# Performance work log

Measured on AMD Instinct MI355X. Metric: run time of the kernel, lower is better.

## Reference

```python
import jax, jax.numpy as jnp
import numpy as np

N_NODES = 25000
N_EDGES = 100000
N_GRAPHS = 1000
DIM = 64
NUM_FEAT = 14
EDGE_FEAT = 4
HIDDEN_EDGE = 128
NUM_OUT = 1
NUM_CONV_STEPS = 3
SET2SET_STEPS = 3
NEG_SLOPE = 0.01


def leaky_relu(x):
    return jnp.where(x > 0, x, NEG_SLOPE * x)


def setup_inputs() -> dict:
    key = jax.random.key(0)
    ks = jax.random.split(key, 24)
    s = lambda fan_in: 1.0 / np.sqrt(fan_in)
    inp = {
        "x": jax.random.normal(ks[0], (N_NODES, NUM_FEAT), dtype=jnp.float32),
        "edge_index": jax.random.randint(ks[1], (2, N_EDGES), 0, N_NODES),
        "edge_attr": jax.random.uniform(ks[2], (N_EDGES, EDGE_FEAT), dtype=jnp.float32),
        "batch": jnp.sort(jax.random.randint(ks[3], (N_NODES,), 0, N_GRAPHS)),
        # lin0
        "lin0_w": jax.random.normal(ks[4], (DIM, NUM_FEAT), dtype=jnp.float32) * s(NUM_FEAT),
        "lin0_b": jnp.zeros((DIM,), dtype=jnp.float32),
        # edge-weight MLP: Linear(4,128) -> LeakyReLU -> Linear(128, DIM*DIM)
        "net_w1": jax.random.normal(ks[5], (HIDDEN_EDGE, EDGE_FEAT), dtype=jnp.float32) * s(EDGE_FEAT),
        "net_b1": jnp.zeros((HIDDEN_EDGE,), dtype=jnp.float32),
        "net_w2": jax.random.normal(ks[6], (DIM * DIM, HIDDEN_EDGE), dtype=jnp.float32) * s(HIDDEN_EDGE),
        "net_b2": jnp.zeros((DIM * DIM,), dtype=jnp.float32),
        # NNConv root weight + bias
        "conv_root": jax.random.normal(ks[7], (DIM, DIM), dtype=jnp.float32) * s(DIM),
        "conv_bias": jnp.zeros((DIM,), dtype=jnp.float32),
        # GRU (single layer), torch gate order r,z,n
        "gru_w_ih": jax.random.normal(ks[8], (3 * DIM, DIM), dtype=jnp.float32) * s(DIM),
        "gru_w_hh": jax.random.normal(ks[9], (3 * DIM, DIM), dtype=jnp.float32) * s(DIM),
        "gru_b_ih": jnp.zeros((3 * DIM,), dtype=jnp.float32),
        "gru_b_hh": jnp.zeros((3 * DIM,), dtype=jnp.float32),
        # Set2Set LSTM: input 2*DIM -> hidden DIM, torch gate order i,f,g,o
        "lstm_w_ih": jax.random.normal(ks[10], (4 * DIM, 2 * DIM), dtype=jnp.float32) * s(2 * DIM),
        "lstm_w_hh": jax.random.normal(ks[11], (4 * DIM, DIM), dtype=jnp.float32) * s(DIM),
        "lstm_b_ih": jnp.zeros((4 * DIM,), dtype=jnp.float32),
        "lstm_b_hh": jnp.zeros((4 * DIM,), dtype=jnp.float32),
        # final linear on [B, 2*DIM]
        "lin_w": jax.random.normal(ks[12], (NUM_OUT, 2 * DIM), dtype=jnp.float32) * s(2 * DIM),
        "lin_b": jnp.zeros((NUM_OUT,), dtype=jnp.float32),
    }
    return inp


def _forward(x, edge_index, edge_attr, batch,
             lin0_w, lin0_b, net_w1, net_b1, net_w2, net_b2,
             conv_root, conv_bias, gru_w_ih, gru_w_hh, gru_b_ih, gru_b_hh,
             lstm_w_ih, lstm_w_hh, lstm_b_ih, lstm_b_hh, lin_w, lin_b):
    src, dst = edge_index[0], edge_index[1]

    out = leaky_relu(x @ lin0_w.T + lin0_b)          # [N, DIM]
    h = out                                          # GRU hidden [N, DIM]

    # edge_attr is constant across conv steps -> dynamic weights computed once
    W_e = (leaky_relu(edge_attr @ net_w1.T + net_b1) @ net_w2.T + net_b2)
    W_e = W_e.reshape(N_EDGES, DIM, DIM)             # [E, DIM, DIM]

    deg = jax.ops.segment_sum(jnp.ones((N_EDGES,), dtype=x.dtype), dst,
                              num_segments=N_NODES)
    inv_deg = jnp.where(deg > 0, 1.0 / jnp.maximum(deg, 1.0), 0.0)[:, None]

    for _ in range(NUM_CONV_STEPS):
        # NNConv: gather -> per-edge matmul -> scatter-mean, plus root term
        msg = jnp.einsum('ed,edo->eo', out[src], W_e)                 # [E, DIM]
        aggr = jax.ops.segment_sum(msg, dst, num_segments=N_NODES) * inv_deg
        m = leaky_relu(aggr + out @ conv_root + conv_bias)
        # single-step GRU (torch equations, gate order r,z,n)
        gi = m @ gru_w_ih.T + gru_b_ih
        gh = h @ gru_w_hh.T + gru_b_hh
        i_r, i_z, i_n = jnp.split(gi, 3, axis=-1)
        h_r, h_z, h_n = jnp.split(gh, 3, axis=-1)
        r = jax.nn.sigmoid(i_r + h_r)
        z = jax.nn.sigmoid(i_z + h_z)
        n = jnp.tanh(i_n + r * h_n)
        h = (1.0 - z) * n + z * h
        out = h

    # Set2Set pooling (processing_steps=3)
    q_star = jnp.zeros((N_GRAPHS, 2 * DIM), dtype=x.dtype)
    hl = jnp.zeros((N_GRAPHS, DIM), dtype=x.dtype)
    cl = jnp.zeros((N_GRAPHS, DIM), dtype=x.dtype)
    for _ in range(SET2SET_STEPS):
        gates = q_star @ lstm_w_ih.T + lstm_b_ih + hl @ lstm_w_hh.T + lstm_b_hh
        gi, gf, gg, go = jnp.split(gates, 4, axis=-1)
        cl = jax.nn.sigmoid(gf) * cl + jax.nn.sigmoid(gi) * jnp.tanh(gg)
        hl = jax.nn.sigmoid(go) * jnp.tanh(cl)
        q = hl                                                         # [B, DIM]
        e = jnp.sum(out * q[batch], axis=-1)                           # [N]
        e_max = jax.ops.segment_max(e, batch, num_segments=N_GRAPHS)
        e_exp = jnp.exp(e - e_max[batch])
        denom = jax.ops.segment_sum(e_exp, batch, num_segments=N_GRAPHS)
        a = e_exp / denom[batch]                                       # segment softmax
        r_read = jax.ops.segment_sum(a[:, None] * out, batch,
                                     num_segments=N_GRAPHS)            # [B, DIM]
        q_star = jnp.concatenate([q, r_read], axis=-1)

    return q_star @ lin_w.T + lin_b                                    # [B, NUM_OUT]


def reference(x, edge_index, edge_attr, batch,
              lin0_w, lin0_b, net_w1, net_b1, net_w2, net_b2,
              conv_root, conv_bias, gru_w_ih, gru_w_hh, gru_b_ih, gru_b_hh,
              lstm_w_ih, lstm_w_hh, lstm_b_ih, lstm_b_hh, lin_w, lin_b):
    return _forward(x, edge_index, edge_attr, batch,
                    lin0_w, lin0_b, net_w1, net_b1, net_w2, net_b2,
                    conv_root, conv_bias, gru_w_ih, gru_w_hh, gru_b_ih, gru_b_hh,
                    lstm_w_ih, lstm_w_hh, lstm_b_ih, lstm_b_hh, lin_w, lin_b)
```

## Files before the change

### kernel.cpp

```cpp
#include <hip/hip_runtime.h>
#include <math.h>

#define N_NODES_C  25000
#define N_EDGES_C  100000
#define N_GRAPHS_C 1000
#define EPB 128

typedef __attribute__((ext_vector_type(8))) _Float16 f16x8;
typedef __attribute__((ext_vector_type(4))) float   f32x4;

__device__ __forceinline__ float lrelu(float x) { return x > 0.f ? x : 0.01f * x; }
__device__ __forceinline__ float sigm(float x)  { return 1.f / (1.f + __expf(-x)); }
__device__ __forceinline__ f32x4 MFH(f16x8 a, f16x8 b, f32x4 c) {
  return __builtin_amdgcn_mfma_f32_16x16x32_f16(a, b, c, 0, 0, 0);
}

__global__ __launch_bounds__(256) void lin0_kernel(const float* __restrict__ x,
                            const float* __restrict__ w, const float* __restrict__ b,
                            float* __restrict__ nodeF) {
  __shared__ float ws[64 * 15];
  __shared__ float bs[64];
  __shared__ float xr[4][16];
  const int tid = threadIdx.x;
  for (int i = tid; i < 896; i += 256) { int o = i / 14, j = i % 14; ws[o * 15 + j] = w[i]; }
  if (tid < 64) bs[tid] = b[tid];
  const int nl = tid >> 6, o = tid & 63;
  const int n = blockIdx.x * 4 + nl;
  if (o < 14 && n < N_NODES_C) xr[nl][o] = x[n * 14 + o];
  __syncthreads();
  if (n < N_NODES_C) {
    float s = bs[o];
#pragma unroll
    for (int j = 0; j < 14; ++j) s += xr[nl][j] * ws[o * 15 + j];
    nodeF[n * 64 + o] = lrelu(s);
  }
}

__global__ void deg_kernel(const int* __restrict__ ei, float* __restrict__ deg) {
  int e = blockIdx.x * blockDim.x + threadIdx.x;
  if (e < N_EDGES_C) atomicAdd(&deg[ei[N_EDGES_C + e]], 1.f);
}

__global__ void invdeg_kernel(float* __restrict__ deg) {
  int n = blockIdx.x * blockDim.x + threadIdx.x;
  if (n < N_NODES_C) { float v = deg[n]; deg[n] = v > 0.f ? 1.f / v : 0.f; }
}

__global__ void goff_kernel(const int* __restrict__ batch, int* __restrict__ goff) {
  int g = blockIdx.x * blockDim.x + threadIdx.x;
  if (g > N_GRAPHS_C) return;
  int lo = 0, hi = N_NODES_C;
  while (lo < hi) { int mid = (lo + hi) >> 1; if (batch[mid] < g) lo = mid + 1; else hi = mid; }
  goff[g] = lo;
}

__global__ void prep_gru_kernel(const float* __restrict__ conv_root,
                                const float* __restrict__ w_ih, const float* __restrict__ w_hh,
                                _Float16* __restrict__ Rtp,
                                _Float16* __restrict__ Wip, _Float16* __restrict__ Whp) {
  int i = blockIdx.x * 256 + threadIdx.x;
  if (i < 12288) {
    int j = i & 7, lane = (i >> 3) & 63, kc = (i >> 9) & 1, t = i >> 10;
    int o = t * 16 + (lane & 15), d = kc * 32 + (lane >> 4) * 8 + j;
    if (i < 4096) Rtp[i] = (_Float16)conv_root[d * 64 + o];
    Wip[i] = (_Float16)w_ih[o * 64 + d];
    Whp[i] = (_Float16)w_hh[o * 64 + d];
  }
}

__global__ __launch_bounds__(256) void prep_w2_kernel(
    const float* __restrict__ net_w2, const float* __restrict__ net_b2,
    _Float16* __restrict__ Wp, _Float16* __restrict__ B2p) {
  int i = blockIdx.x * 256 + threadIdx.x;
  {
    int j = i & 7, lane = (i >> 3) & 63, q = (i >> 9) & 3, p = (i >> 11) & 1;
    int oh = (i >> 12) & 1, d = i >> 13;
    int kci = q >> 1, ob = q & 1;
    int col = lane & 15, kg = lane >> 4;
    int o = oh * 32 + ob * 16 + col, h = (p * 2 + kci) * 32 + kg * 8 + j;
    Wp[i] = (_Float16)net_w2[((size_t)d * 64 + o) * 128 + h];
  }
  if (i < 4096) {
    int j = i & 7, lane = (i >> 3) & 63, kc2 = (i >> 9) & 1, ob = (i >> 10) & 1, oh = (i >> 11) & 1;
    int col = lane & 15, kg = lane >> 4;
    int o = oh * 32 + ob * 16 + col, d = kc2 * 32 + kg * 8 + j;
    B2p[i] = (_Float16)net_b2[d * 64 + o];
  }
}

__global__ __launch_bounds__(256, 3) void msg_kernel(
    const float* __restrict__ nodef,
    const int*   __restrict__ ei,
    const float* __restrict__ eattr,
    const float* __restrict__ net_w1,
    const float* __restrict__ net_b1,
    const _Float16* __restrict__ Wp,
    const _Float16* __restrict__ B2p,
    float* __restrict__ aggr)
{
  __shared__ _Float16 xs[64 * EPB];
  __shared__ _Float16 xsT[EPB * 64];
  __shared__ float    w1s[128 * 5];

  const int tid = threadIdx.x;
  const int e0 = blockIdx.x * EPB;

  if (tid < 128) {
    float4 wv = *(const float4*)(net_w1 + tid * 4);
    w1s[tid * 5 + 0] = wv.x; w1s[tid * 5 + 1] = wv.y;
    w1s[tid * 5 + 2] = wv.z; w1s[tid * 5 + 3] = wv.w;
    w1s[tid * 5 + 4] = net_b1[tid];
  }
  {
    const int e = tid >> 1, dh = (tid & 1) * 32;
    int ge = e0 + e;
    const int esw = (e & 7) << 3;
#pragma unroll
    for (int jb = 0; jb < 4; ++jb) {
      int d = dh + jb * 8;
      float4 v0, v1;
      if (ge < N_EDGES_C) {
        const float4* nf4 = (const float4*)(nodef + (size_t)ei[ge] * 64 + d);
        v0 = nf4[0]; v1 = nf4[1];
      } else {
        v0 = make_float4(0.f, 0.f, 0.f, 0.f); v1 = v0;
      }
      f16x8 pk;
      pk[0] = (_Float16)v0.x; pk[1] = (_Float16)v0.y; pk[2] = (_Float16)v0.z; pk[3] = (_Float16)v0.w;
      pk[4] = (_Float16)v1.x; pk[5] = (_Float16)v1.y; pk[6] = (_Float16)v1.z; pk[7] = (_Float16)v1.w;
      *(f16x8*)&xsT[e * 64 + (d ^ esw)] = pk;
#pragma unroll
      for (int j = 0; j < 8; ++j) xs[(d + j) * EPB + e] = pk[j];
    }
  }

  const int lane = tid & 63, wv = tid >> 6;
  const int e0w = (wv & 1) * 64;
  const int oh  = wv >> 1;
  const int col = lane & 15;
  const int kg  = lane >> 4;
  const int swz = (col & 7) << 3;

  __syncthreads();

  f32x4 acc[4][2];
#pragma unroll
  for (int eb = 0; eb < 4; ++eb) { acc[eb][0] = 0.f; acc[eb][1] = 0.f; }
#pragma unroll
  for (int ob = 0; ob < 2; ++ob)
#pragma unroll
    for (int kc2 = 0; kc2 < 2; ++kc2) {
      f16x8 b2f = *(const f16x8*)(B2p + oh * 2048 + ob * 1024 + kc2 * 512 + lane * 8);
#pragma unroll
      for (int eb = 0; eb < 4; ++eb) {
        f16x8 xf = *(const f16x8*)&xsT[(e0w + eb * 16 + col) * 64 + ((kc2 * 32 + kg * 8) ^ swz)];
        acc[eb][ob] = MFH(xf, b2f, acc[eb][ob]);
      }
    }

  const _Float16* wp_base = Wp + oh * 4096 + lane * 8;
#pragma unroll 1
  for (int p = 0; p < 2; ++p) {
    f16x8 Af[4][2];
    {
      float4 at[4];
#pragma unroll
      for (int eb = 0; eb < 4; ++eb) {
        int ge = e0 + e0w + eb * 16 + col;
        at[eb] = (ge < N_EDGES_C) ? *(const float4*)(eattr + (size_t)ge * 4)
                                  : make_float4(0.f, 0.f, 0.f, 0.f);
      }
#pragma unroll
      for (int kci = 0; kci < 2; ++kci) {
        float4 wr[8]; float wb[8];
#pragma unroll
        for (int j = 0; j < 8; ++j) {
          int hq = (p * 2 + kci) * 32 + kg * 8 + j;
          wr[j] = *(const float4*)&w1s[hq * 5];
          wb[j] = w1s[hq * 5 + 4];
        }
#pragma unroll
        for (int eb = 0; eb < 4; ++eb) {
          f16x8 F;
#pragma unroll
          for (int j = 0; j < 8; ++j) {
            float a = wb[j] + at[eb].x * wr[j].x + at[eb].y * wr[j].y
                            + at[eb].z * wr[j].z + at[eb].w * wr[j].w;
            F[j] = (_Float16)lrelu(a);
          }
          Af[eb][kci] = F;
        }
      }
    }

    const _Float16* wp_p = wp_base + p * 2048;
    f16x8 B0[4], B1[4];
#define LOADB(BUF, dd)                                                   \
  {                                                                      \
    const _Float16* b_ = wp_p + (size_t)(dd) * 8192;                     \
    BUF[0] = *(const f16x8*)(b_);                                        \
    BUF[1] = *(const f16x8*)(b_ + 512);                                  \
    BUF[2] = *(const f16x8*)(b_ + 1024);                                 \
    BUF[3] = *(const f16x8*)(b_ + 1536);                                 \
  }
#define SLAB(BUF, dd)                                                    \
  {                                                                      \
    _Pragma("unroll")                                                    \
    for (int eb = 0; eb < 4; ++eb) {                                     \
      unsigned int xu = *(const unsigned short*)&xs[(dd) * EPB + e0w + eb * 16 + col]; \
      unsigned int xr_ = (xu << 16) | xu;                                \
      union { unsigned int u[4]; f16x8 v; } X;                           \
      X.u[0] = xr_; X.u[1] = xr_; X.u[2] = xr_; X.u[3] = xr_;            \
      _Pragma("unroll")                                                  \
      for (int kci = 0; kci < 2; ++kci) {                                \
        f16x8 U = Af[eb][kci] * X.v;                                     \
        acc[eb][0] = MFH(U, BUF[kci * 2 + 0], acc[eb][0]);               \
        acc[eb][1] = MFH(U, BUF[kci * 2 + 1], acc[eb][1]);               \
      }                                                                  \
    }                                                                    \
  }
    LOADB(B0, 0);
#pragma unroll 1
    for (int d = 0; d < 64; d += 2) {
      LOADB(B1, d + 1);
      SLAB(B0, d);
      if (d + 2 < 64) LOADB(B0, d + 2);
      SLAB(B1, d + 1);
    }
#undef LOADB
#undef SLAB
  }

  const int o0w = oh * 32;
#pragma unroll
  for (int eb = 0; eb < 4; ++eb) {
#pragma unroll
    for (int r = 0; r < 4; ++r) {
      int e = e0w + eb * 16 + kg * 4 + r;
      int ge = e0 + e;
      if (ge < N_EDGES_C) {
        int dn = ei[N_EDGES_C + ge];
        atomicAdd(&aggr[(size_t)dn * 64 + o0w + col],      acc[eb][0][r]);
        atomicAdd(&aggr[(size_t)dn * 64 + o0w + 16 + col], acc[eb][1][r]);
      }
    }
  }
}

__global__ __launch_bounds__(256) void node_update_kernel(
    float* __restrict__ aggr, const float* __restrict__ invdeg,
    const _Float16* __restrict__ Rtp, const _Float16* __restrict__ Wip,
    const _Float16* __restrict__ Whp,
    const float* __restrict__ conv_bias,
    const float* __restrict__ b_ih, const float* __restrict__ b_hh,
    float* __restrict__ nodeF)
{
  __shared__ _Float16 ms[4][16 * 64];

  const int tid = threadIdx.x, lane = tid & 63, wv = tid >> 6;
  const int col = lane & 15, kg = lane >> 4;
  const int nwb = blockIdx.x * 64 + wv * 16;

  int arow = nwb + col; if (arow >= N_NODES_C) arow = N_NODES_C - 1;
  f16x8 nf[2];
#pragma unroll
  for (int kc = 0; kc < 2; ++kc) {
    f32x4 v0 = *(const f32x4*)(nodeF + (size_t)arow * 64 + kc * 32 + kg * 8);
    f32x4 v1 = *(const f32x4*)(nodeF + (size_t)arow * 64 + kc * 32 + kg * 8 + 4);
    f16x8 F;
#pragma unroll
    for (int j = 0; j < 4; ++j) { F[j] = (_Float16)v0[j]; F[4 + j] = (_Float16)v1[j]; }
    nf[kc] = F;
  }

  f32x4 racc[4];
#pragma unroll
  for (int t = 0; t < 4; ++t) racc[t] = conv_bias[t * 16 + col];
#pragma unroll
  for (int t = 0; t < 4; ++t)
#pragma unroll
    for (int kc = 0; kc < 2; ++kc)
      racc[t] = MFH(nf[kc], *(const f16x8*)(Rtp + t * 1024 + kc * 512 + lane * 8), racc[t]);

  float invd[4]; int nrow[4];
#pragma unroll
  for (int r = 0; r < 4; ++r) {
    int nn = nwb + kg * 4 + r; nrow[r] = nn;
    invd[r] = (nn < N_NODES_C) ? invdeg[nn] : 0.f;
  }
#pragma unroll
  for (int t = 0; t < 4; ++t) {
#pragma unroll
    for (int r = 0; r < 4; ++r) {
      int nn = nrow[r];
      float ag = 0.f;
      if (nn < N_NODES_C) {
        size_t idx = (size_t)nn * 64 + t * 16 + col;
        ag = aggr[idx];
        aggr[idx] = 0.f;
      }
      float mval = lrelu(ag * invd[r] + racc[t][r]);
      int nl = kg * 4 + r;
      int dsw = (t * 16 + col) ^ ((nl & 7) << 3);
      ms[wv][nl * 64 + dsw] = (_Float16)mval;
    }
  }
  __syncthreads();

  f16x8 ma[2];
#pragma unroll
  for (int kc = 0; kc < 2; ++kc)
    ma[kc] = *(const f16x8*)&ms[wv][col * 64 + ((kc * 32 + kg * 8) ^ ((col & 7) << 3))];

  f32x4 gi[12], gh[12];
#pragma unroll
  for (int t = 0; t < 12; ++t) { gi[t] = b_ih[t * 16 + col]; gh[t] = b_hh[t * 16 + col]; }
#pragma unroll
  for (int t = 0; t < 12; ++t)
#pragma unroll
    for (int kc = 0; kc < 2; ++kc) {
      gi[t] = MFH(ma[kc], *(const f16x8*)(Wip + t * 1024 + kc * 512 + lane * 8), gi[t]);
      gh[t] = MFH(nf[kc], *(const f16x8*)(Whp + t * 1024 + kc * 512 + lane * 8), gh[t]);
    }

#pragma unroll
  for (int t = 0; t < 4; ++t) {
#pragma unroll
    for (int r = 0; r < 4; ++r) {
      int nn = nrow[r];
      if (nn >= N_NODES_C) continue;
      size_t idx = (size_t)nn * 64 + t * 16 + col;
      float hv = nodeF[idx];
      float rr = sigm(gi[t][r] + gh[t][r]);
      float zz = sigm(gi[t + 4][r] + gh[t + 4][r]);
      float nv = tanhf(gi[t + 8][r] + rr * gh[t + 8][r]);
      nodeF[idx] = (1.f - zz) * nv + zz * hv;
    }
  }
}

__global__ __launch_bounds__(64) void set2set_kernel(
    const float* __restrict__ nodeF, const int* __restrict__ goff,
    const float* __restrict__ w_ih, const float* __restrict__ w_hh,
    const float* __restrict__ b_ih, const float* __restrict__ b_hh,
    const float* __restrict__ lw, const float* __restrict__ lb,
    float* __restrict__ ebuf, float* __restrict__ dout)
{
  const int g = blockIdx.x, t = threadIdx.x;
  __shared__ float qs[128], hs[64];
  float hl = 0.f, cl = 0.f;
  qs[t] = 0.f; qs[64 + t] = 0.f;
  const int s0 = goff[g], s1 = goff[g + 1];

  for (int step = 0; step < 3; ++step) {
    hs[t] = hl;
    __syncthreads();
    float gv[4];
#pragma unroll
    for (int k = 0; k < 4; ++k) {
      float s = b_ih[k * 64 + t] + b_hh[k * 64 + t];
      const float4* wi4 = (const float4*)(w_ih + (k * 64 + t) * 128);
#pragma unroll 8
      for (int j = 0; j < 32; ++j) {
        float4 w = wi4[j];
        s += qs[4 * j] * w.x + qs[4 * j + 1] * w.y + qs[4 * j + 2] * w.z + qs[4 * j + 3] * w.w;
      }
      const float4* wh4 = (const float4*)(w_hh + (k * 64 + t) * 64);
#pragma unroll 8
      for (int j = 0; j < 16; ++j) {
        float4 w = wh4[j];
        s += hs[4 * j] * w.x + hs[4 * j + 1] * w.y + hs[4 * j + 2] * w.z + hs[4 * j + 3] * w.w;
      }
      gv[k] = s;
    }
    cl = sigm(gv[1]) * cl + sigm(gv[0]) * tanhf(gv[2]);
    hl = sigm(gv[3]) * tanhf(cl);
    const float qv = hl;

    float emax = -3.0e38f;
    for (int n = s0; n < s1; ++n) {
      float p = nodeF[n * 64 + t] * qv;
#pragma unroll
      for (int off = 32; off > 0; off >>= 1) p += __shfl_down(p, off);
      float en = __shfl(p, 0);
      if (t == 0) ebuf[n] = en;
      emax = fmaxf(emax, en);
    }
    __syncthreads();
    float lsum = 0.f;
    for (int n = s0 + t; n < s1; n += 64) {
      float ex = __expf(ebuf[n] - emax);
      ebuf[n] = ex;
      lsum += ex;
    }
#pragma unroll
    for (int off = 32; off > 0; off >>= 1) lsum += __shfl_down(lsum, off);
    float denom = __shfl(lsum, 0);
    __syncthreads();
    float r = 0.f;
    for (int n = s0; n < s1; ++n) r += ebuf[n] * nodeF[n * 64 + t];
    if (s1 > s0) r /= denom;
    qs[t] = qv; qs[64 + t] = r;
  }
  __syncthreads();
  float s = qs[t] * lw[t] + qs[64 + t] * lw[64 + t];
#pragma unroll
  for (int off = 32; off > 0; off >>= 1) s += __shfl_down(s, off);
  if (t == 0) dout[g] = s + lb[0];
}

extern "C" void kernel_launch(void* const* d_in, const int* in_sizes, int n_in,
                              void* d_out, int out_size, void* d_ws, size_t ws_size,
                              hipStream_t stream) {
  const float* x         = (const float*)d_in[0];
  const int*   ei        = (const int*)  d_in[1];
  const float* eattr     = (const float*)d_in[2];
  const int*   batch     = (const int*)  d_in[3];
  const float* lin0_w    = (const float*)d_in[4];
  const float* lin0_b    = (const float*)d_in[5];
  const float* net_w1    = (const float*)d_in[6];
  const float* net_b1    = (const float*)d_in[7];
  const float* net_w2    = (const float*)d_in[8];
  const float* net_b2    = (const float*)d_in[9];
  const float* conv_root = (const float*)d_in[10];
  const float* conv_bias = (const float*)d_in[11];
  const float* gru_w_ih  = (const float*)d_in[12];
  const float* gru_w_hh  = (const float*)d_in[13];
  const float* gru_b_ih  = (const float*)d_in[14];
  const float* gru_b_hh  = (const float*)d_in[15];
  const float* lstm_w_ih = (const float*)d_in[16];
  const float* lstm_w_hh = (const float*)d_in[17];
  const float* lstm_b_ih = (const float*)d_in[18];
  const float* lstm_b_hh = (const float*)d_in[19];
  const float* lin_w     = (const float*)d_in[20];
  const float* lin_b     = (const float*)d_in[21];

  float* ws    = (float*)d_ws;
  float* nodeF = ws;
  float* aggr  = nodeF + 1600000;
  float* deg   = aggr + 1600000;
  float* ebuf  = deg + 25000;
  int*   goff  = (int*)(ebuf + 25000);
  _Float16* Rtp = (_Float16*)(goff + 1024);
  _Float16* Wip = Rtp + 4096;
  _Float16* Whp = Wip + 12288;
  _Float16* Wp  = Whp + 12288;
  _Float16* B2p = Wp + 524288;

  hipMemsetAsync(deg, 0, 25000 * sizeof(float), stream);
  hipMemsetAsync(aggr, 0, 1600000 * sizeof(float), stream);

  lin0_kernel<<<(N_NODES_C + 3) / 4, 256, 0, stream>>>(x, lin0_w, lin0_b, nodeF);
  deg_kernel<<<(N_EDGES_C + 255) / 256, 256, 0, stream>>>(ei, deg);
  invdeg_kernel<<<(N_NODES_C + 255) / 256, 256, 0, stream>>>(deg);
  goff_kernel<<<(N_GRAPHS_C + 256) / 256, 256, 0, stream>>>(batch, goff);
  prep_gru_kernel<<<48, 256, 0, stream>>>(conv_root, gru_w_ih, gru_w_hh, Rtp, Wip, Whp);
  prep_w2_kernel<<<2048, 256, 0, stream>>>(net_w2, net_b2, Wp, B2p);

  for (int step = 0; step < 3; ++step) {
    msg_kernel<<<(N_EDGES_C + EPB - 1) / EPB, 256, 0, stream>>>(
        nodeF, ei, eattr, net_w1, net_b1, Wp, B2p, aggr);
    node_update_kernel<<<(N_NODES_C + 63) / 64, 256, 0, stream>>>(
        aggr, deg, Rtp, Wip, Whp, conv_bias, gru_b_ih, gru_b_hh, nodeF);
  }

  set2set_kernel<<<N_GRAPHS_C, 64, 0, stream>>>(
      nodeF, goff, lstm_w_ih, lstm_w_hh, lstm_b_ih, lstm_b_hh, lin_w, lin_b, ebuf, (float*)d_out);
}
```

Measured before the change: 618.3 us.

## Drop transposed xs buffer, read node features as vectors from xsT in message kernel

Removes the second shared-memory copy of gathered node features (xs) and instead loads eight features per edge at once from the swizzled xsT buffer, broadcasting each half via byte permute. This halves the shared memory per block, removes the scalar scatter stores, and replaces per-d scalar LDS loads with one vector load per eight d. The launch bound is raised to 4 blocks per SM to exploit the lower LDS use, which tightens the register budget and risks spills.

After: 602.2 us. -2.6%, faster.

```diff
diff --git a/kernel.cpp b/kernel.cpp
--- a/kernel.cpp
+++ b/kernel.cpp
@@ -7,6 +7,7 @@
 #define EPB 128
 
 typedef __attribute__((ext_vector_type(8))) _Float16 f16x8;
+typedef __attribute__((ext_vector_type(2))) _Float16 f16x2;
 typedef __attribute__((ext_vector_type(4))) float   f32x4;
 
 __device__ __forceinline__ float lrelu(float x) { return x > 0.f ? x : 0.01f * x; }
@@ -88,7 +89,7 @@
   }
 }
 
-__global__ __launch_bounds__(256, 3) void msg_kernel(
+__global__ __launch_bounds__(256, 4) void msg_kernel(
     const float* __restrict__ nodef,
     const int*   __restrict__ ei,
     const float* __restrict__ eattr,
@@ -98,7 +99,6 @@
     const _Float16* __restrict__ B2p,
     float* __restrict__ aggr)
 {
-  __shared__ _Float16 xs[64 * EPB];
   __shared__ _Float16 xsT[EPB * 64];
   __shared__ float    w1s[128 * 5];
 
@@ -129,8 +129,6 @@
       pk[0] = (_Float16)v0.x; pk[1] = (_Float16)v0.y; pk[2] = (_Float16)v0.z; pk[3] = (_Float16)v0.w;
       pk[4] = (_Float16)v1.x; pk[5] = (_Float16)v1.y; pk[6] = (_Float16)v1.z; pk[7] = (_Float16)v1.w;
       *(f16x8*)&xsT[e * 64 + (d ^ esw)] = pk;
-#pragma unroll
-      for (int j = 0; j < 8; ++j) xs[(d + j) * EPB + e] = pk[j];
     }
   }
 
@@ -194,7 +192,7 @@
     }
 
     const _Float16* wp_p = wp_base + p * 2048;
-    f16x8 B0[4], B1[4];
+    f16x8 Bb[2][4];
 #define LOADB(BUF, dd)                                                   \
   {                                                                      \
     const _Float16* b_ = wp_p + (size_t)(dd) * 8192;                     \
@@ -203,32 +201,36 @@
     BUF[2] = *(const f16x8*)(b_ + 1024);                                 \
     BUF[3] = *(const f16x8*)(b_ + 1536);                                 \
   }
-#define SLAB(BUF, dd)                                                    \
-  {                                                                      \
-    _Pragma("unroll")                                                    \
-    for (int eb = 0; eb < 4; ++eb) {                                     \
-      unsigned int xu = *(const unsigned short*)&xs[(dd) * EPB + e0w + eb * 16 + col]; \
-      unsigned int xr_ = (xu << 16) | xu;                                \
-      union { unsigned int u[4]; f16x8 v; } X;                           \
-      X.u[0] = xr_; X.u[1] = xr_; X.u[2] = xr_; X.u[3] = xr_;            \
-      _Pragma("unroll")                                                  \
-      for (int kci = 0; kci < 2; ++kci) {                                \
-        f16x8 U = Af[eb][kci] * X.v;                                     \
-        acc[eb][0] = MFH(U, BUF[kci * 2 + 0], acc[eb][0]);               \
-        acc[eb][1] = MFH(U, BUF[kci * 2 + 1], acc[eb][1]);               \
-      }                                                                  \
-    }                                                                    \
-  }
-    LOADB(B0, 0);
+    LOADB(Bb[0], 0);
 #pragma unroll 1
-    for (int d = 0; d < 64; d += 2) {
-      LOADB(B1, d + 1);
-      SLAB(B0, d);
-      if (d + 2 < 64) LOADB(B0, d + 2);
-      SLAB(B1, d + 1);
+    for (int d8 = 0; d8 < 64; d8 += 8) {
+      union { f16x8 v; unsigned u[4]; } XV[4];
+#pragma unroll
+      for (int eb = 0; eb < 4; ++eb)
+        XV[eb].v = *(const f16x8*)&xsT[(e0w + eb * 16 + col) * 64 + (d8 ^ swz)];
+#pragma unroll
+      for (int j = 0; j < 8; ++j) {
+        int d = d8 + j;
+        if (d < 63) LOADB(Bb[(j + 1) & 1], d + 1);
+        const f16x8* B = Bb[j & 1];
+#pragma unroll
+        for (int eb = 0; eb < 4; ++eb) {
+          unsigned dw = XV[eb].u[j >> 1];
+          unsigned xd = __builtin_amdgcn_perm(dw, dw, (j & 1) ? 0x03020302u : 0x01000100u);
+          f16x2 x2; { union { unsigned u; f16x2 h; } c; c.u = xd; x2 = c.h; }
+#pragma unroll
+          for (int kci = 0; kci < 2; ++kci) {
+            union { f16x8 v; f16x2 p[4]; } af, Uu;
+            af.v = Af[eb][kci];
+#pragma unroll
+            for (int q = 0; q < 4; ++q) Uu.p[q] = af.p[q] * x2;
+            acc[eb][0] = MFH(Uu.v, B[kci * 2 + 0], acc[eb][0]);
+            acc[eb][1] = MFH(Uu.v, B[kci * 2 + 1], acc[eb][1]);
+          }
+        }
+      }
     }
 #undef LOADB
-#undef SLAB
   }
 
   const int o0w = oh * 32;
```
